# Performance work log

Measured on AMD Instinct MI355X. Metric: run time of the kernel, lower is better.

The kernel has to match this reference:

```python
import jax, jax.numpy as jnp
import numpy as np

SIGMA = 0.001
EPS_LOG = 1e-12
EPS_COS = 1e-8


def setup_inputs() -> dict:
    key = jax.random.key(0)
    k1, k2, k3, k4 = jax.random.split(key, 4)
    B, T, K, S, d = 32, 512, 8, 8, 300
    center_pos = jax.random.randint(k1, (B,), 0, T)
    query_token_ids = jax.random.randint(k2, (B, T), 0, 30000)
    center_sense_embeddings = jax.random.normal(k3, (B, K, d), dtype=jnp.float32)
    context_sense_embeddings = jax.random.normal(k4, (B, T - 1, S, d), dtype=jnp.float32)
    return {
        'center_pos': center_pos,
        'query_token_ids': query_token_ids,
        'center_sense_embeddings': center_sense_embeddings,
        'context_sense_embeddings': context_sense_embeddings,
    }


def reference(center_pos, query_token_ids, center_sense_embeddings, context_sense_embeddings):
    B, T = query_token_ids.shape
    d = center_sense_embeddings.shape[-1]
    # v: mean over senses of context tokens -> [B, C, d], C = T-1
    v = context_sense_embeddings.mean(axis=-2)
    # a: scaled dot between center senses and context vectors -> [B, C, K]
    a = jnp.einsum('bkd,bcd->bck', center_sense_embeddings, v) / jnp.sqrt(jnp.float32(d))
    # context positions: skip the center position (vectorized form of the per-batch loop)
    i = jnp.arange(T - 1)  # [C]
    ctx_pos = i[None, :] + (i[None, :] >= center_pos[:, None])  # [B, C]
    w = jnp.exp(-jnp.abs(ctx_pos - center_pos[:, None]).astype(jnp.float32) / SIGMA)
    logw = jnp.log(jnp.maximum(w, EPS_LOG))  # [B, C]
    alpha = jax.nn.softmax(a + logw[:, :, None], axis=1)  # softmax over context positions
    m = jnp.einsum('bck,bcd->bkd', alpha, v)  # [B, K, d]
    # cosine similarity along d (torch semantics: clamp each norm by eps)
    num = jnp.sum(center_sense_embeddings * m, axis=-1)
    n1 = jnp.linalg.norm(center_sense_embeddings, axis=-1)
    n2 = jnp.linalg.norm(m, axis=-1)
    s = num / (jnp.maximum(n1, EPS_COS) * jnp.maximum(n2, EPS_COS))  # [B, K]
    q = jax.nn.softmax(s, axis=-1)
    idx = jnp.argmax(q, axis=-1)  # [B]
    pooled = jnp.take_along_axis(center_sense_embeddings, idx[:, None, None], axis=1)[:, 0, :]  # [B, d]
    return pooled, q
```

## Files before the change

### kernel.cpp

```cpp
#include <hip/hip_runtime.h>

#define NB 32
#define NC 511
#define NK 8
#define NS 8
#define ND 300
#define ND4 75
#define NCG 16
#define GPB 8
#define EPS_COS 1e-8f


typedef float nfloat4 __attribute__((ext_vector_type(4)));

__device__ __forceinline__ void n4add(nfloat4& a, const nfloat4& b) { a += b; }

__global__ __launch_bounds__(256, 4) void k_vam(const float* __restrict__ ctx,
                                                const float* __restrict__ cen,
                                                float* __restrict__ part) {
    const int b    = blockIdx.x >> 4;
    const int cg   = blockIdx.x & 15;
    const int w    = threadIdx.x >> 6;
    const int lane = threadIdx.x & 63;
    const int t    = threadIdx.x;
    const int i0 = lane;
    const int i1 = lane + 64;
    const bool has1  = (i1 < ND4);
    const bool hasd1 = (t < ND - 256);

    __shared__ float vl[4][ND4 * 4 + 4];
    __shared__ float al[4][NK];

    const nfloat4* cen4 = (const nfloat4*)cen + (size_t)b * NK * ND4;

    float acc0[NK] = {};
    float acc1[NK] = {};

    const int cbase0 = cg * 32;

    for (int g = 0; g < GPB; ++g) {
        const int cbase = cbase0 + g * 4;
        const int cn = min(4, NC - cbase);
        const int c = cbase + w;

        if (c < NC) {
            const nfloat4* ctx4 =
                (const nfloat4*)ctx + (size_t)(b * NC + c) * NS * ND4;

            nfloat4 X[NS];
#pragma unroll
            for (int s = 0; s < NS; ++s)
                X[s] = __builtin_nontemporal_load(&ctx4[s * ND4 + i0]);
            nfloat4 Y[NS] = {};
            if (has1) {
#pragma unroll
                for (int s = 0; s < NS; ++s)
                    Y[s] = __builtin_nontemporal_load(&ctx4[s * ND4 + i1]);
            }

            n4add(X[0], X[1]); n4add(X[2], X[3]); n4add(X[4], X[5]); n4add(X[6], X[7]);
            n4add(X[0], X[2]); n4add(X[4], X[6]);
            n4add(X[0], X[4]);
            n4add(Y[0], Y[1]); n4add(Y[2], Y[3]); n4add(Y[4], Y[5]); n4add(Y[6], Y[7]);
            n4add(Y[0], Y[2]); n4add(Y[4], Y[6]);
            n4add(Y[0], Y[4]);
            const float inv = 0.125f;
            nfloat4 s0 = X[0] * inv;
            nfloat4 s1 = Y[0] * inv;

            ((nfloat4*)vl[w])[i0] = s0;
            if (has1) ((nfloat4*)vl[w])[i1] = s1;

            float pk[NK];
#pragma unroll
            for (int k = 0; k < NK; ++k) {
                nfloat4 ca = cen4[k * ND4 + i0];
                float p = ca.x * s0.x + ca.y * s0.y + ca.z * s0.z + ca.w * s0.w;
                if (has1) {
                    nfloat4 cb = cen4[k * ND4 + i1];
                    p += cb.x * s1.x + cb.y * s1.y + cb.z * s1.z + cb.w * s1.w;
                }
                pk[k] = p;
            }

            const bool b0 = (lane & 1) != 0;
            float r[4];
#pragma unroll
            for (int j = 0; j < 4; ++j) {
                float keep = b0 ? pk[2 * j + 1] : pk[2 * j];
                float send = b0 ? pk[2 * j]     : pk[2 * j + 1];
                r[j] = keep + __shfl_xor(send, 1);
            }
            const bool b1 = (lane & 2) != 0;
            float q0, q1;
            { float keep = b1 ? r[1] : r[0]; float send = b1 ? r[0] : r[1];
              q0 = keep + __shfl_xor(send, 2); }
            { float keep = b1 ? r[3] : r[2]; float send = b1 ? r[2] : r[3];
              q1 = keep + __shfl_xor(send, 2); }
            const bool b2 = (lane & 4) != 0;
            float u;
            { float keep = b2 ? q1 : q0; float send = b2 ? q0 : q1;
              u = keep + __shfl_xor(send, 4); }
            u += __shfl_xor(u, 8);
            u += __shfl_xor(u, 16);
            u += __shfl_xor(u, 32);

            if (lane < NK) {
                const float scale = 0.057735026919f;
                al[w][lane] = __expf(u * scale);
            }
        }
        __syncthreads();

        for (int cc = 0; cc < cn; ++cc) {
            float vv0 = vl[cc][t];
#pragma unroll
            for (int k = 0; k < NK; ++k) acc0[k] += al[cc][k] * vv0;
        }
        if (hasd1) {
            for (int cc = 0; cc < cn; ++cc) {
                float vv1 = vl[cc][256 + t];
#pragma unroll
                for (int k = 0; k < NK; ++k) acc1[k] += al[cc][k] * vv1;
            }
        }
        __syncthreads();
        asm volatile("" ::: "memory");
    }

#pragma unroll
    for (int k = 0; k < NK; ++k) {
        float* pp = part + (((size_t)(b * NK + k)) * NCG + cg) * ND;
        pp[t] = acc0[k];
        if (hasd1) pp[256 + t] = acc1[k];
    }
}

__global__ __launch_bounds__(512) void k_fin2(const float* __restrict__ part,
                                              const float* __restrict__ cen,
                                              float* __restrict__ out) {
    const int b    = blockIdx.x;
    const int w    = threadIdx.x >> 6;
    const int lane = threadIdx.x & 63;
    __shared__ float sred[NK];
    __shared__ int bidx;

    const float* pp = part + ((size_t)b * NK + w) * NCG * ND;
    const float* cp = cen + (size_t)(b * NK + w) * ND;
    float num = 0.f, n1 = 0.f, n2 = 0.f;
    for (int d = lane; d < ND; d += 64) {
        float mval = 0.f;
#pragma unroll
        for (int cg = 0; cg < NCG; ++cg) mval += pp[cg * ND + d];
        float cv = cp[d];
        num += cv * mval; n1 += cv * cv; n2 += mval * mval;
    }
#pragma unroll
    for (int off = 32; off; off >>= 1) {
        num += __shfl_down(num, off);
        n1  += __shfl_down(n1, off);
        n2  += __shfl_down(n2, off);
    }
    if (lane == 0) {
        float denom = fmaxf(sqrtf(n1), EPS_COS) * fmaxf(sqrtf(n2), EPS_COS);
        sred[w] = num / denom;
    }
    __syncthreads();

    if (threadIdx.x == 0) {
        float mx = sred[0];
#pragma unroll
        for (int k = 1; k < NK; ++k) mx = fmaxf(mx, sred[k]);
        float e[NK], sum = 0.f;
#pragma unroll
        for (int k = 0; k < NK; ++k) { e[k] = __expf(sred[k] - mx); sum += e[k]; }
        float invs = 1.f / sum;
        int best = 0; float bv = sred[0];
#pragma unroll
        for (int k = 1; k < NK; ++k) if (sred[k] > bv) { bv = sred[k]; best = k; }
#pragma unroll
        for (int k = 0; k < NK; ++k)
            out[(size_t)NB * ND + b * NK + k] = e[k] * invs;
        bidx = best;
    }
    __syncthreads();

    const float* src = cen + (size_t)(b * NK + bidx) * ND;
    for (int idx = threadIdx.x; idx < ND; idx += 512)
        out[(size_t)b * ND + idx] = src[idx];
}

extern "C" void kernel_launch(void* const* d_in, const int* in_sizes, int n_in,
                              void* d_out, int out_size, void* d_ws, size_t ws_size,
                              hipStream_t stream) {
    const float* cen = (const float*)d_in[2];
    const float* ctx = (const float*)d_in[3];
    float* out = (float*)d_out;

    float* part = (float*)d_ws;

    k_vam<<<dim3(NB * NCG), dim3(256), 0, stream>>>(ctx, cen, part);
    k_fin2<<<dim3(NB), dim3(512), 0, stream>>>(part, cen, out);
}
```

Baseline: 238.7 us.

## Prefetch next context group into registers and split blocks finer

Software-pipelines the context loads in k_vam: the next group's 8 sense vectors are issued into registers right after the current group has been reduced, so global loads overlap with the dot-product, shuffle reduction and accumulation work. Each block now covers 16 context positions instead of 32 (NCG doubles to 32, GPB halves to 4), which doubles the grid and the partial buffer that k_fin2 has to sum. __syncthreads is replaced by raw s_barrier plus an explicit lgkmcnt wait, so the barriers no longer drain the outstanding vmem prefetch. The prefetch keeps about 16 float4 values live across iterations, which raises register pressure under the 4-waves launch bound. k_fin2 is untouched and relies on NCG to read all 32 partials.

```diff
diff --git a/kernel.cpp b/kernel.cpp
--- a/kernel.cpp
+++ b/kernel.cpp
@@ -6,20 +6,32 @@
 #define NS 8
 #define ND 300
 #define ND4 75
-#define NCG 16
-#define GPB 8
+#define NCG 32
+#define GPB 4
 #define EPS_COS 1e-8f
 
 
 typedef float nfloat4 __attribute__((ext_vector_type(4)));
 
 __device__ __forceinline__ void n4add(nfloat4& a, const nfloat4& b) { a += b; }
+
+#define ISSUE_LOADS(cptr)                                                     \
+    do {                                                                      \
+        _Pragma("unroll")                                                     \
+        for (int s = 0; s < NS; ++s)                                          \
+            X[s] = __builtin_nontemporal_load(&(cptr)[s * ND4 + i0]);         \
+        if (has1) {                                                           \
+            _Pragma("unroll")                                                 \
+            for (int s = 0; s < NS; ++s)                                      \
+                Y[s] = __builtin_nontemporal_load(&(cptr)[s * ND4 + i1]);     \
+        }                                                                     \
+    } while (0)
 
 __global__ __launch_bounds__(256, 4) void k_vam(const float* __restrict__ ctx,
                                                 const float* __restrict__ cen,
                                                 float* __restrict__ part) {
-    const int b    = blockIdx.x >> 4;
-    const int cg   = blockIdx.x & 15;
+    const int b    = blockIdx.x >> 5;
+    const int cg   = blockIdx.x & 31;
     const int w    = threadIdx.x >> 6;
     const int lane = threadIdx.x & 63;
     const int t    = threadIdx.x;
@@ -36,28 +48,24 @@
     float acc0[NK] = {};
     float acc1[NK] = {};
 
-    const int cbase0 = cg * 32;
+    const int cbase0 = cg * (GPB * 4);
+    int  c  = cbase0 + w;
+    bool cv = (c < NC);
+
+    nfloat4 X[NS];
+    nfloat4 Y[NS] = {};
+
+    if (cv) {
+        const nfloat4* p = (const nfloat4*)ctx + (size_t)(b * NC + c) * NS * ND4;
+        ISSUE_LOADS(p);
+    }
 
     for (int g = 0; g < GPB; ++g) {
         const int cbase = cbase0 + g * 4;
         const int cn = min(4, NC - cbase);
-        const int c = cbase + w;
-
-        if (c < NC) {
-            const nfloat4* ctx4 =
-                (const nfloat4*)ctx + (size_t)(b * NC + c) * NS * ND4;
-
-            nfloat4 X[NS];
-#pragma unroll
-            for (int s = 0; s < NS; ++s)
-                X[s] = __builtin_nontemporal_load(&ctx4[s * ND4 + i0]);
-            nfloat4 Y[NS] = {};
-            if (has1) {
-#pragma unroll
-                for (int s = 0; s < NS; ++s)
-                    Y[s] = __builtin_nontemporal_load(&ctx4[s * ND4 + i1]);
-            }
-
+
+        nfloat4 s0 = {}, s1 = {};
+        if (cv) {
             n4add(X[0], X[1]); n4add(X[2], X[3]); n4add(X[4], X[5]); n4add(X[6], X[7]);
             n4add(X[0], X[2]); n4add(X[4], X[6]);
             n4add(X[0], X[4]);
@@ -65,9 +73,19 @@
             n4add(Y[0], Y[2]); n4add(Y[4], Y[6]);
             n4add(Y[0], Y[4]);
             const float inv = 0.125f;
-            nfloat4 s0 = X[0] * inv;
-            nfloat4 s1 = Y[0] * inv;
-
+            s0 = X[0] * inv;
+            s1 = Y[0] * inv;
+        }
+
+        const bool cv_next = (g + 1 < GPB) && (cbase0 + (g + 1) * 4 + w < NC);
+        if (cv_next) {
+            const int cnx = cbase0 + (g + 1) * 4 + w;
+            const nfloat4* p =
+                (const nfloat4*)ctx + (size_t)(b * NC + cnx) * NS * ND4;
+            ISSUE_LOADS(p);
+        }
+
+        if (cv) {
             ((nfloat4*)vl[w])[i0] = s0;
             if (has1) ((nfloat4*)vl[w])[i1] = s1;
 
@@ -110,7 +128,9 @@
                 al[w][lane] = __expf(u * scale);
             }
         }
-        __syncthreads();
+
+        asm volatile("s_waitcnt lgkmcnt(0)" ::: "memory");
+        __builtin_amdgcn_s_barrier();
 
         for (int cc = 0; cc < cn; ++cc) {
             float vv0 = vl[cc][t];
@@ -124,8 +144,12 @@
                 for (int k = 0; k < NK; ++k) acc1[k] += al[cc][k] * vv1;
             }
         }
-        __syncthreads();
+
         asm volatile("" ::: "memory");
+        __builtin_amdgcn_s_barrier();
+
+        cv = cv_next;
+        c += 4;
     }
 
 #pragma unroll
```

Measured after the change: 270.4 us. 1.13x slower.

## Double-buffer context groups to overlap next-group loads with accumulation

Applied to the files above, without the earlier changes.

Restructures k_vam into a software pipeline. The global loads for the next group of four context positions are issued before the current group's weighted accumulation, and the mean and attention results go to a ping-pong shared buffer. This removes one barrier per iteration and lets memory latency hide behind the FMA work. It raises register pressure, so launch bounds drop from 4 to 2 blocks per CU, which may cut the occupancy that was hiding latency before.

```diff
diff --git a/kernel.cpp b/kernel.cpp
--- a/kernel.cpp
+++ b/kernel.cpp
@@ -15,7 +15,7 @@
 
 __device__ __forceinline__ void n4add(nfloat4& a, const nfloat4& b) { a += b; }
 
-__global__ __launch_bounds__(256, 4) void k_vam(const float* __restrict__ ctx,
+__global__ __launch_bounds__(256, 2) void k_vam(const float* __restrict__ ctx,
                                                 const float* __restrict__ cen,
                                                 float* __restrict__ part) {
     const int b    = blockIdx.x >> 4;
@@ -28,36 +28,122 @@
     const bool has1  = (i1 < ND4);
     const bool hasd1 = (t < ND - 256);
 
-    __shared__ float vl[4][ND4 * 4 + 4];
-    __shared__ float al[4][NK];
+    __shared__ float vl[2][4][ND4 * 4 + 4];
+    __shared__ float al[2][4][NK];
 
     const nfloat4* cen4 = (const nfloat4*)cen + (size_t)b * NK * ND4;
 
     float acc0[NK] = {};
     float acc1[NK] = {};
 
-    const int cbase0 = cg * 32;
+    const int cbase0 = cg * (GPB * 4);
+
+    nfloat4 X[NS];
+    nfloat4 Y[NS] = {};
+
+    {
+        const int c = cbase0 + w;
+        const nfloat4* ctx4 =
+            (const nfloat4*)ctx + (size_t)(b * NC + c) * NS * ND4;
+#pragma unroll
+        for (int s = 0; s < NS; ++s)
+            X[s] = __builtin_nontemporal_load(&ctx4[s * ND4 + i0]);
+        if (has1) {
+#pragma unroll
+            for (int s = 0; s < NS; ++s)
+                Y[s] = __builtin_nontemporal_load(&ctx4[s * ND4 + i1]);
+        }
+        n4add(X[0], X[1]); n4add(X[2], X[3]); n4add(X[4], X[5]); n4add(X[6], X[7]);
+        n4add(X[0], X[2]); n4add(X[4], X[6]);
+        n4add(X[0], X[4]);
+        n4add(Y[0], Y[1]); n4add(Y[2], Y[3]); n4add(Y[4], Y[5]); n4add(Y[6], Y[7]);
+        n4add(Y[0], Y[2]); n4add(Y[4], Y[6]);
+        n4add(Y[0], Y[4]);
+        const float inv = 0.125f;
+        nfloat4 s0 = X[0] * inv;
+        nfloat4 s1 = Y[0] * inv;
+
+        ((nfloat4*)vl[0][w])[i0] = s0;
+        if (has1) ((nfloat4*)vl[0][w])[i1] = s1;
+
+        float pk[NK];
+#pragma unroll
+        for (int k = 0; k < NK; ++k) {
+            nfloat4 ca = cen4[k * ND4 + i0];
+            float p = ca.x * s0.x + ca.y * s0.y + ca.z * s0.z + ca.w * s0.w;
+            if (has1) {
+                nfloat4 cb = cen4[k * ND4 + i1];
+                p += cb.x * s1.x + cb.y * s1.y + cb.z * s1.z + cb.w * s1.w;
+            }
+            pk[k] = p;
+        }
+        const bool b0 = (lane & 1) != 0;
+        float r[4];
+#pragma unroll
+        for (int j = 0; j < 4; ++j) {
+            float keep = b0 ? pk[2 * j + 1] : pk[2 * j];
+            float send = b0 ? pk[2 * j]     : pk[2 * j + 1];
+            r[j] = keep + __shfl_xor(send, 1);
+        }
+        const bool b1 = (lane & 2) != 0;
+        float q0, q1;
+        { float keep = b1 ? r[1] : r[0]; float send = b1 ? r[0] : r[1];
+          q0 = keep + __shfl_xor(send, 2); }
+        { float keep = b1 ? r[3] : r[2]; float send = b1 ? r[2] : r[3];
+          q1 = keep + __shfl_xor(send, 2); }
+        const bool b2 = (lane & 4) != 0;
+        float u;
+        { float keep = b2 ? q1 : q0; float send = b2 ? q0 : q1;
+          u = keep + __shfl_xor(send, 4); }
+        u += __shfl_xor(u, 8);
+        u += __shfl_xor(u, 16);
+        u += __shfl_xor(u, 32);
+        if (lane < NK) {
+            const float scale = 0.057735026919f;
+            al[0][w][lane] = __expf(u * scale);
+        }
+    }
 
     for (int g = 0; g < GPB; ++g) {
-        const int cbase = cbase0 + g * 4;
-        const int cn = min(4, NC - cbase);
-        const int c = cbase + w;
-
-        if (c < NC) {
+        __syncthreads();
+
+        const int buf = g & 1;
+        const int nbf = buf ^ 1;
+        const int cn  = min(4, NC - (cbase0 + g * 4));
+
+        const bool cvn = (g + 1 < GPB) && (cbase0 + (g + 1) * 4 + w < NC);
+        if (cvn) {
+            const int cnx = cbase0 + (g + 1) * 4 + w;
             const nfloat4* ctx4 =
-                (const nfloat4*)ctx + (size_t)(b * NC + c) * NS * ND4;
-
-            nfloat4 X[NS];
+                (const nfloat4*)ctx + (size_t)(b * NC + cnx) * NS * ND4;
 #pragma unroll
             for (int s = 0; s < NS; ++s)
                 X[s] = __builtin_nontemporal_load(&ctx4[s * ND4 + i0]);
-            nfloat4 Y[NS] = {};
             if (has1) {
 #pragma unroll
                 for (int s = 0; s < NS; ++s)
                     Y[s] = __builtin_nontemporal_load(&ctx4[s * ND4 + i1]);
             }
-
+        }
+
+        for (int cc = 0; cc < cn; ++cc) {
+            nfloat4 a0 = ((const nfloat4*)al[buf][cc])[0];
+            nfloat4 a1 = ((const nfloat4*)al[buf][cc])[1];
+            float vv0 = vl[buf][cc][t];
+            acc0[0] += a0.x * vv0; acc0[1] += a0.y * vv0;
+            acc0[2] += a0.z * vv0; acc0[3] += a0.w * vv0;
+            acc0[4] += a1.x * vv0; acc0[5] += a1.y * vv0;
+            acc0[6] += a1.z * vv0; acc0[7] += a1.w * vv0;
+            if (hasd1) {
+                float vv1 = vl[buf][cc][256 + t];
+                acc1[0] += a0.x * vv1; acc1[1] += a0.y * vv1;
+                acc1[2] += a0.z * vv1; acc1[3] += a0.w * vv1;
+                acc1[4] += a1.x * vv1; acc1[5] += a1.y * vv1;
+                acc1[6] += a1.z * vv1; acc1[7] += a1.w * vv1;
+            }
+        }
+
+        if (cvn) {
             n4add(X[0], X[1]); n4add(X[2], X[3]); n4add(X[4], X[5]); n4add(X[6], X[7]);
             n4add(X[0], X[2]); n4add(X[4], X[6]);
             n4add(X[0], X[4]);
@@ -68,8 +154,8 @@
             nfloat4 s0 = X[0] * inv;
             nfloat4 s1 = Y[0] * inv;
 
-            ((nfloat4*)vl[w])[i0] = s0;
-            if (has1) ((nfloat4*)vl[w])[i1] = s1;
+            ((nfloat4*)vl[nbf][w])[i0] = s0;
+            if (has1) ((nfloat4*)vl[nbf][w])[i1] = s1;
 
             float pk[NK];
 #pragma unroll
@@ -82,7 +168,6 @@
                 }
                 pk[k] = p;
             }
-
             const bool b0 = (lane & 1) != 0;
             float r[4];
 #pragma unroll
@@ -104,27 +189,11 @@
             u += __shfl_xor(u, 8);
             u += __shfl_xor(u, 16);
             u += __shfl_xor(u, 32);
-
             if (lane < NK) {
                 const float scale = 0.057735026919f;
-                al[w][lane] = __expf(u * scale);
-            }
-        }
-        __syncthreads();
-
-        for (int cc = 0; cc < cn; ++cc) {
-            float vv0 = vl[cc][t];
-#pragma unroll
-            for (int k = 0; k < NK; ++k) acc0[k] += al[cc][k] * vv0;
-        }
-        if (hasd1) {
-            for (int cc = 0; cc < cn; ++cc) {
-                float vv1 = vl[cc][256 + t];
-#pragma unroll
-                for (int k = 0; k < NK; ++k) acc1[k] += al[cc][k] * vv1;
-            }
-        }
-        __syncthreads();
+                al[nbf][w][lane] = __expf(u * scale);
+            }
+        }
         asm volatile("" ::: "memory");
     }
 
```

Result: faster. 233.8 us (-2.0%).

## Software-pipeline context loads with double-buffered registers and shared memory

Applied to the files above, without the earlier changes.

The per-group loop in k_vam becomes a two-stage pipeline. While the current group is accumulated into the outputs, global loads for a later group of context rows are already in flight, using two register sets (XA/XB, YA/YB) and double-buffered shared `vl`/`al` arrays. The attention weights are now read from shared memory as float4 vectors, and launch bounds relax from 4 to 2 blocks per SM so the extra live registers fit. The aim is to hide global load latency in a latency-bound streaming kernel, at the cost of higher register pressure and lower occupancy.

```diff
diff --git a/kernel.cpp b/kernel.cpp
--- a/kernel.cpp
+++ b/kernel.cpp
@@ -15,7 +15,90 @@
 
 __device__ __forceinline__ void n4add(nfloat4& a, const nfloat4& b) { a += b; }
 
-__global__ __launch_bounds__(256, 4) void k_vam(const float* __restrict__ ctx,
+#define ISSUE(Xs, Ys, cidx)                                                   \
+    do {                                                                      \
+        const nfloat4* ctx4_ =                                                \
+            (const nfloat4*)ctx + (size_t)(b * NC + (cidx)) * NS * ND4;       \
+        _Pragma("unroll")                                                     \
+        for (int s = 0; s < NS; ++s)                                          \
+            Xs[s] = __builtin_nontemporal_load(&ctx4_[s * ND4 + i0]);         \
+        if (has1) {                                                           \
+            _Pragma("unroll")                                                 \
+            for (int s = 0; s < NS; ++s)                                      \
+                Ys[s] = __builtin_nontemporal_load(&ctx4_[s * ND4 + i1]);     \
+        }                                                                     \
+    } while (0)
+
+#define PHASE1(Xs, Ys, BUF)                                                   \
+    do {                                                                      \
+        n4add(Xs[0], Xs[1]); n4add(Xs[2], Xs[3]);                             \
+        n4add(Xs[4], Xs[5]); n4add(Xs[6], Xs[7]);                             \
+        n4add(Xs[0], Xs[2]); n4add(Xs[4], Xs[6]);                             \
+        n4add(Xs[0], Xs[4]);                                                  \
+        n4add(Ys[0], Ys[1]); n4add(Ys[2], Ys[3]);                             \
+        n4add(Ys[4], Ys[5]); n4add(Ys[6], Ys[7]);                             \
+        n4add(Ys[0], Ys[2]); n4add(Ys[4], Ys[6]);                             \
+        n4add(Ys[0], Ys[4]);                                                  \
+        nfloat4 s0 = Xs[0] * 0.125f;                                          \
+        nfloat4 s1 = Ys[0] * 0.125f;                 \
+        ((nfloat4*)vl[BUF][w])[i0] = s0;                                      \
+        if (has1) ((nfloat4*)vl[BUF][w])[i1] = s1;                            \
+        float pk[NK];                                                         \
+        _Pragma("unroll")                                                     \
+        for (int k = 0; k < NK; ++k) {                                        \
+            nfloat4 ca = cen4[k * ND4 + i0];                                  \
+            float p = ca.x*s0.x + ca.y*s0.y + ca.z*s0.z + ca.w*s0.w;          \
+            if (has1) {                                                       \
+                nfloat4 cb = cen4[k * ND4 + i1];                              \
+                p += cb.x*s1.x + cb.y*s1.y + cb.z*s1.z + cb.w*s1.w;           \
+            }                                                                 \
+            pk[k] = p;                                                        \
+        }                                                                     \
+        const bool bb0 = (lane & 1) != 0;                                     \
+        float rr[4];                                                          \
+        _Pragma("unroll")                                                     \
+        for (int j = 0; j < 4; ++j) {                                         \
+            float keep = bb0 ? pk[2*j+1] : pk[2*j];                           \
+            float send = bb0 ? pk[2*j]   : pk[2*j+1];                         \
+            rr[j] = keep + __shfl_xor(send, 1);                               \
+        }                                                                     \
+        const bool bb1 = (lane & 2) != 0;                                     \
+        float qq0, qq1;                                                       \
+        { float keep = bb1 ? rr[1] : rr[0]; float send = bb1 ? rr[0] : rr[1]; \
+          qq0 = keep + __shfl_xor(send, 2); }                                 \
+        { float keep = bb1 ? rr[3] : rr[2]; float send = bb1 ? rr[2] : rr[3]; \
+          qq1 = keep + __shfl_xor(send, 2); }                                 \
+        const bool bb2 = (lane & 4) != 0;                                     \
+        float uu;                                                             \
+        { float keep = bb2 ? qq1 : qq0; float send = bb2 ? qq0 : qq1;         \
+          uu = keep + __shfl_xor(send, 4); }                                  \
+        uu += __shfl_xor(uu, 8);                                              \
+        uu += __shfl_xor(uu, 16);                                             \
+        uu += __shfl_xor(uu, 32);                                             \
+        if (lane < NK) al[BUF][w][lane] = __expf(uu * 0.057735026919f);       \
+    } while (0)
+
+#define PHASE2(BUF, CN)                                                       \
+    do {                                                                      \
+        for (int cc = 0; cc < (CN); ++cc) {                                   \
+            nfloat4 a0 = ((const nfloat4*)al[BUF][cc])[0];                    \
+            nfloat4 a1 = ((const nfloat4*)al[BUF][cc])[1];                    \
+            float vv0 = vl[BUF][cc][t];                                       \
+            acc0[0] += a0.x * vv0; acc0[1] += a0.y * vv0;                     \
+            acc0[2] += a0.z * vv0; acc0[3] += a0.w * vv0;                     \
+            acc0[4] += a1.x * vv0; acc0[5] += a1.y * vv0;                     \
+            acc0[6] += a1.z * vv0; acc0[7] += a1.w * vv0;                     \
+            if (hasd1) {                                                      \
+                float vv1 = vl[BUF][cc][256 + t];                             \
+                acc1[0] += a0.x * vv1; acc1[1] += a0.y * vv1;                 \
+                acc1[2] += a0.z * vv1; acc1[3] += a0.w * vv1;                 \
+                acc1[4] += a1.x * vv1; acc1[5] += a1.y * vv1;                 \
+                acc1[6] += a1.z * vv1; acc1[7] += a1.w * vv1;                 \
+            }                                                                 \
+        }                                                                     \
+    } while (0)
+
+__global__ __launch_bounds__(256, 2) void k_vam(const float* __restrict__ ctx,
                                                 const float* __restrict__ cen,
                                                 float* __restrict__ part) {
     const int b    = blockIdx.x >> 4;
@@ -28,103 +111,46 @@
     const bool has1  = (i1 < ND4);
     const bool hasd1 = (t < ND - 256);
 
-    __shared__ float vl[4][ND4 * 4 + 4];
-    __shared__ float al[4][NK];
+    __shared__ float vl[2][4][ND4 * 4 + 4];
+    __shared__ float al[2][4][NK];
 
     const nfloat4* cen4 = (const nfloat4*)cen + (size_t)b * NK * ND4;
 
     float acc0[NK] = {};
     float acc1[NK] = {};
 
-    const int cbase0 = cg * 32;
-
-    for (int g = 0; g < GPB; ++g) {
-        const int cbase = cbase0 + g * 4;
-        const int cn = min(4, NC - cbase);
-        const int c = cbase + w;
-
-        if (c < NC) {
-            const nfloat4* ctx4 =
-                (const nfloat4*)ctx + (size_t)(b * NC + c) * NS * ND4;
-
-            nfloat4 X[NS];
-#pragma unroll
-            for (int s = 0; s < NS; ++s)
-                X[s] = __builtin_nontemporal_load(&ctx4[s * ND4 + i0]);
-            nfloat4 Y[NS] = {};
-            if (has1) {
-#pragma unroll
-                for (int s = 0; s < NS; ++s)
-                    Y[s] = __builtin_nontemporal_load(&ctx4[s * ND4 + i1]);
-            }
-
-            n4add(X[0], X[1]); n4add(X[2], X[3]); n4add(X[4], X[5]); n4add(X[6], X[7]);
-            n4add(X[0], X[2]); n4add(X[4], X[6]);
-            n4add(X[0], X[4]);
-            n4add(Y[0], Y[1]); n4add(Y[2], Y[3]); n4add(Y[4], Y[5]); n4add(Y[6], Y[7]);
-            n4add(Y[0], Y[2]); n4add(Y[4], Y[6]);
-            n4add(Y[0], Y[4]);
-            const float inv = 0.125f;
-            nfloat4 s0 = X[0] * inv;
-            nfloat4 s1 = Y[0] * inv;
-
-            ((nfloat4*)vl[w])[i0] = s0;
-            if (has1) ((nfloat4*)vl[w])[i1] = s1;
-
-            float pk[NK];
-#pragma unroll
-            for (int k = 0; k < NK; ++k) {
-                nfloat4 ca = cen4[k * ND4 + i0];
-                float p = ca.x * s0.x + ca.y * s0.y + ca.z * s0.z + ca.w * s0.w;
-                if (has1) {
-                    nfloat4 cb = cen4[k * ND4 + i1];
-                    p += cb.x * s1.x + cb.y * s1.y + cb.z * s1.z + cb.w * s1.w;
-                }
-                pk[k] = p;
-            }
-
-            const bool b0 = (lane & 1) != 0;
-            float r[4];
-#pragma unroll
-            for (int j = 0; j < 4; ++j) {
-                float keep = b0 ? pk[2 * j + 1] : pk[2 * j];
-                float send = b0 ? pk[2 * j]     : pk[2 * j + 1];
-                r[j] = keep + __shfl_xor(send, 1);
-            }
-            const bool b1 = (lane & 2) != 0;
-            float q0, q1;
-            { float keep = b1 ? r[1] : r[0]; float send = b1 ? r[0] : r[1];
-              q0 = keep + __shfl_xor(send, 2); }
-            { float keep = b1 ? r[3] : r[2]; float send = b1 ? r[2] : r[3];
-              q1 = keep + __shfl_xor(send, 2); }
-            const bool b2 = (lane & 4) != 0;
-            float u;
-            { float keep = b2 ? q1 : q0; float send = b2 ? q0 : q1;
-              u = keep + __shfl_xor(send, 4); }
-            u += __shfl_xor(u, 8);
-            u += __shfl_xor(u, 16);
-            u += __shfl_xor(u, 32);
-
-            if (lane < NK) {
-                const float scale = 0.057735026919f;
-                al[w][lane] = __expf(u * scale);
-            }
-        }
+    const int cbase0 = cg * (GPB * 4);
+
+    nfloat4 XA[NS], XB[NS];
+    nfloat4 YA[NS] = {}, YB[NS] = {};
+
+    ISSUE(XA, YA, cbase0 + w);
+    ISSUE(XB, YB, cbase0 + 4 + w);
+    PHASE1(XA, YA, 0);
+
+    for (int gp = 0; gp < GPB; gp += 2) {
         __syncthreads();
-
-        for (int cc = 0; cc < cn; ++cc) {
-            float vv0 = vl[cc][t];
-#pragma unroll
-            for (int k = 0; k < NK; ++k) acc0[k] += al[cc][k] * vv0;
-        }
-        if (hasd1) {
-            for (int cc = 0; cc < cn; ++cc) {
-                float vv1 = vl[cc][256 + t];
-#pragma unroll
-                for (int k = 0; k < NK; ++k) acc1[k] += al[cc][k] * vv1;
-            }
-        }
+        if (gp + 2 < GPB) {
+            const int cpre = cbase0 + (gp + 2) * 4 + w;
+            if (cpre < NC) ISSUE(XA, YA, cpre);
+        }
+        PHASE2(0, min(4, NC - (cbase0 + gp * 4)));
+        {
+            const int cnx = cbase0 + (gp + 1) * 4 + w;
+            if (cnx < NC) PHASE1(XB, YB, 1);
+        }
+        asm volatile("" ::: "memory");
+
         __syncthreads();
+        if (gp + 3 < GPB) {
+            const int cpre = cbase0 + (gp + 3) * 4 + w;
+            if (cpre < NC) ISSUE(XB, YB, cpre);
+        }
+        PHASE2(1, min(4, NC - (cbase0 + (gp + 1) * 4)));
+        if (gp + 2 < GPB) {
+            const int cnx = cbase0 + (gp + 2) * 4 + w;
+            if (cnx < NC) PHASE1(XA, YA, 0);
+        }
         asm volatile("" ::: "memory");
     }
 
```

Result: no change. 239.6 us (+0.4%).
